# Kernel optimization log

Hardware: AMD Instinct MI355X
Metric: run time of the kernel (lower is better)

Reference implementation:

```python
import jax, jax.numpy as jnp
import numpy as np
from jax import lax

DIM = 512
HEADS = 8
N = 2048
B = 4
EPS = 1e-12  # torch F.normalize eps


def setup_inputs() -> dict:
    key = jax.random.key(0)
    ks = jax.random.split(key, 8)
    s = 0.02
    return {
        "x": jax.random.normal(ks[0], (B, DIM, N), jnp.float32),
        "w_qkv": jax.random.normal(ks[1], (3 * DIM, DIM, 1), jnp.float32) * s,
        "b_qkv": jax.random.normal(ks[2], (3 * DIM,), jnp.float32) * s,
        "w_dw": jax.random.normal(ks[3], (3 * DIM, 1, 3), jnp.float32) * s,
        "b_dw": jax.random.normal(ks[4], (3 * DIM,), jnp.float32) * s,
        "w_po": jax.random.normal(ks[5], (DIM, DIM, 1), jnp.float32) * s,
        "b_po": jax.random.normal(ks[6], (DIM,), jnp.float32) * s,
        "temperature": jnp.ones((HEADS, 1, 1), jnp.float32),
    }


def _l2norm(x, axis):
    n = jnp.sqrt(jnp.sum(x * x, axis=axis, keepdims=True))
    return x / jnp.maximum(n, EPS)


def reference(x, w_qkv, b_qkv, w_dw, b_dw, w_po, b_po, temperature):
    b, c, n = x.shape
    ch = c // HEADS
    # 1x1 conv (pointwise)
    qkv = jnp.einsum('oc,bcn->bon', w_qkv[:, :, 0], x) + b_qkv[None, :, None]
    # depthwise conv k=3, pad=1
    qkv = lax.conv_general_dilated(
        qkv, w_dw, window_strides=(1,), padding=[(1, 1)],
        dimension_numbers=('NCH', 'OIH', 'NCH'),
        feature_group_count=3 * c) + b_dw[None, :, None]
    q, k, v = jnp.split(qkv, 3, axis=1)  # each [b, c, n]
    q = q.reshape(b, HEADS, ch, n)
    k = k.reshape(b, HEADS, ch, n)
    v = v.reshape(b, HEADS, ch, n)
    q = _l2norm(q, axis=-1)          # normalize over sequence axis
    k = _l2norm(k, axis=1)           # normalize over HEAD axis (faithful)
    # attn[i, j] = sum_c k[c, i] * q[c, j]  -> [b, h, n, n]
    attn = jnp.einsum('bhci,bhcj->bhij', k, q) * temperature[None]
    attn = jax.nn.softmax(attn, axis=-1)
    out = jnp.einsum('bhij,bhcj->bhic', attn, v)  # [b, h, n, ch]
    out = out.transpose(0, 1, 3, 2).reshape(b, c, n)  # b (head c) n
    out = jnp.einsum('oc,bcn->bon', w_po[:, :, 0], out) + b_po[None, :, None]
    return out
```

## Files before the change

kernel.cpp:

```cpp
#include <hip/hip_runtime.h>
#include <hip/hip_bf16.h>

#define BATCH 4
#define DIM 512
#define HEADS 8
#define CH 64
#define SEQ 2048
#define C3 1536
#define L2EPS 1e-12f

typedef float f32x4 __attribute__((ext_vector_type(4)));
typedef short s16x8 __attribute__((ext_vector_type(8)));
typedef short s16x4 __attribute__((ext_vector_type(4)));
typedef unsigned short ushort_t;

static __device__ __forceinline__ unsigned bfpair(float a, float b) {
  unsigned ua = __builtin_bit_cast(unsigned, a);
  unsigned ub = __builtin_bit_cast(unsigned, b);
  ua = (ua + 0x7FFFu + ((ua >> 16) & 1u)) >> 16;
  ub = (ub + 0x7FFFu + ((ub >> 16) & 1u)) >> 16;
  return ua | (ub << 16);
}

static __device__ __forceinline__ unsigned cvtpk(float lo, float hi) {
  unsigned r;
  asm("v_cvt_pk_bf16_f32 %0, %1, %2" : "=v"(r) : "v"(lo), "v"(hi));
  return r;
}

static __device__ __forceinline__ float fexp2(float x) {
  float r;
  asm("v_exp_f32 %0, %1" : "=v"(r) : "v"(x));
  return r;
}

static __device__ __forceinline__ void gl_lds16(const void* g, void* l) {
  __builtin_amdgcn_global_load_lds(
      (const __attribute__((address_space(1))) unsigned int*)g,
      (__attribute__((address_space(3))) unsigned int*)l, 16, 0, 0);
}

__global__ __launch_bounds__(256) void wprep(
    const float* __restrict__ wq, const float* __restrict__ wp,
    unsigned* __restrict__ wqb, unsigned* __restrict__ wpb) {
  const int id = blockIdx.x * 256 + threadIdx.x;
  const float* src;
  unsigned* dst;
  int rid;
  if (id < 1536 * 256) { src = wq; dst = wqb; rid = id; }
  else                 { src = wp; dst = wpb; rid = id - 1536 * 256; }
  const int m = rid >> 8, dcol = rid & 255;
  const int chunk = dcol >> 5, dw = dcol & 31;
  const int sdw = chunk * 32 + (dw ^ (4 * (m & 7)));
  const float* s = src + (size_t)m * 512 + 2 * sdw;
  dst[rid] = bfpair(s[0], s[1]);
}

__global__ __launch_bounds__(256) void xpose_bf16(
    const float* __restrict__ x, unsigned* __restrict__ xbt) {
  __shared__ unsigned T[64][32];
  const int b = blockIdx.z;
  const int k0 = blockIdx.y * 64;
  const int n0 = blockIdx.x * 64;
  const int nl = threadIdx.x & 63;
  const int dwg = threadIdx.x >> 6;
  const float* xb = x + ((size_t)b * DIM + k0) * SEQ + n0 + nl;
#pragma unroll
  for (int dd = 0; dd < 8; ++dd) {
    const int dw = dwg * 8 + dd;
    const float v0 = xb[(size_t)(2 * dw) * SEQ];
    const float v1 = xb[(size_t)(2 * dw + 1) * SEQ];
    T[nl][dw ^ (4 * (nl & 7))] = bfpair(v0, v1);
  }
  __syncthreads();
#pragma unroll
  for (int rep = 0; rep < 8; ++rep) {
    const int id = rep * 256 + threadIdx.x;
    const int row = id >> 5, dw = id & 31;
    xbt[((size_t)b * SEQ + n0 + row) * 256 + (k0 >> 1) + dw] = T[row][dw];
  }
}

__global__ __launch_bounds__(256) void gemm_mfma_bf16(
    const ushort_t* __restrict__ Wb, const ushort_t* __restrict__ Bt,
    const float* __restrict__ bias, float* __restrict__ Y,
    int M, int N) {
  __shared__ __align__(16) char lds[32768];
  char* As = lds;
  char* Bs = lds + 16384;
  const int b = blockIdx.z;
  const int m0 = blockIdx.y * 128, n0 = blockIdx.x * 128;
  const int t = threadIdx.x, w = t >> 6, lane = t & 63;
  const int l15 = lane & 15, g = lane >> 4;
  const int key = 16 * (l15 & 7);
  const int wm = (w >> 1) * 64, wn = (w & 1) * 64;

  const int rsub = lane >> 3;
  const int csub = (lane & 7) * 8;

  f32x4 acc[4][4] = {};

  const ushort_t* Ag0 = Wb + (size_t)(m0 + 32 * w + rsub) * 512 + csub;
  const ushort_t* Bg0 = Bt + ((size_t)b * N + n0 + 32 * w + rsub) * 512 + csub;
  char* Al0 = As + (32 * w) * 128;
  char* Bl0 = Bs + (32 * w) * 128;

  for (int kc = 0; kc < 8; ++kc) {
    const int ko64 = kc * 64;
#pragma unroll
    for (int ri = 0; ri < 4; ++ri) {
      gl_lds16(Ag0 + (size_t)(8 * ri) * 512 + ko64, Al0 + ri * 1024);
      gl_lds16(Bg0 + (size_t)(8 * ri) * 512 + ko64, Bl0 + ri * 1024);
    }
    __syncthreads();
    const char* Abase = As + (wm + l15) * 128;
    const char* Bbase = Bs + (wn + l15) * 128;
#pragma unroll
    for (int ks = 0; ks < 2; ++ks) {
      const int ko = (64 * ks + 16 * g) ^ key;
      s16x8 af[4], bf[4];
#pragma unroll
      for (int mf = 0; mf < 4; ++mf) af[mf] = *(const s16x8*)(Abase + mf * 2048 + ko);
#pragma unroll
      for (int nf = 0; nf < 4; ++nf) bf[nf] = *(const s16x8*)(Bbase + nf * 2048 + ko);
#pragma unroll
      for (int mf = 0; mf < 4; ++mf)
#pragma unroll
        for (int nf = 0; nf < 4; ++nf)
          acc[mf][nf] = __builtin_amdgcn_mfma_f32_16x16x32_bf16(
              af[mf], bf[nf], acc[mf][nf], 0, 0, 0);
    }
    __syncthreads();
  }

#pragma unroll
  for (int mf = 0; mf < 4; ++mf) {
#pragma unroll
    for (int rg = 0; rg < 4; ++rg) {
      const int m = m0 + wm + 16 * mf + 4 * g + rg;
      const float bv = bias[m];
      float* yp = Y + ((size_t)b * M + m) * N + n0 + wn + l15;
#pragma unroll
      for (int nf = 0; nf < 4; ++nf)
        yp[16 * nf] = acc[mf][nf][rg] + bv;
    }
  }
}

__global__ __launch_bounds__(256) void dwconv2(
    const float* __restrict__ pre, const float* __restrict__ wdw,
    const float* __restrict__ bdw, float* __restrict__ qkv,
    unsigned* __restrict__ vb, float* __restrict__ rq) {
  __shared__ float red[4];
  const int row = blockIdx.x;
  const int o = row % C3;
  const int b = row / C3;
  const int n0 = threadIdx.x * 8;
  const float* src = pre + (size_t)row * SEQ + n0;
  float4 m0 = *(const float4*)src;
  float4 m1 = *(const float4*)(src + 4);
  const float left  = (n0 > 0) ? src[-1] : 0.f;
  const float right = (n0 < SEQ - 8) ? src[8] : 0.f;
  const float w0 = wdw[o * 3 + 0], w1 = wdw[o * 3 + 1], w2 = wdw[o * 3 + 2];
  const float bv = bdw[o];
  const float mid[8] = {m0.x, m0.y, m0.z, m0.w, m1.x, m1.y, m1.z, m1.w};
  const float lf[8]  = {left, m0.x, m0.y, m0.z, m0.w, m1.x, m1.y, m1.z};
  const float rt[8]  = {m0.y, m0.z, m0.w, m1.x, m1.y, m1.z, m1.w, right};
  float y[8];
#pragma unroll
  for (int u = 0; u < 8; ++u) y[u] = w0 * lf[u] + w1 * mid[u] + w2 * rt[u] + bv;

  if (o < 2 * DIM) {
    float* dst = qkv + (size_t)row * SEQ + n0;
    *(float4*)dst = make_float4(y[0], y[1], y[2], y[3]);
    *(float4*)(dst + 4) = make_float4(y[4], y[5], y[6], y[7]);
    if (o < DIM) {
      float s = 0.f;
#pragma unroll
      for (int u = 0; u < 8; ++u) s += y[u] * y[u];
#pragma unroll
      for (int off = 32; off > 0; off >>= 1) s += __shfl_down(s, off);
      if ((threadIdx.x & 63) == 0) red[threadIdx.x >> 6] = s;
      __syncthreads();
      if (threadIdx.x == 0) {
        const float tv = red[0] + red[1] + red[2] + red[3];
        rq[b * DIM + o] = 1.0f / fmaxf(sqrtf(tv), L2EPS);
      }
    }
  } else {
    const int oc = o - 2 * DIM;
    const int h = oc >> 6, cc = oc & 63;
    const int bh = b * 8 + h;
    const int jt = n0 >> 6, d0 = (n0 & 63) >> 1;
    uint4 pk;
    pk.x = bfpair(y[0], y[1]); pk.y = bfpair(y[2], y[3]);
    pk.z = bfpair(y[4], y[5]); pk.w = bfpair(y[6], y[7]);
    *(uint4*)&vb[((size_t)(bh * 32 + jt) * 64 + cc) * 32 +
                 (d0 ^ (4 * (cc & 7)))] = pk;
  }
}

__global__ __launch_bounds__(256) void knorm_kernel(
    const float* __restrict__ qkv, float* __restrict__ rk) {
  const int idx = blockIdx.x * 256 + threadIdx.x;
  const int n = idx & (SEQ - 1);
  const int cc = (idx >> 11) & 63;
  const int b = idx >> 17;
  const float* base = qkv + ((size_t)b * C3 + DIM + cc) * SEQ + n;
  float s = 0.f;
#pragma unroll
  for (int h = 0; h < HEADS; ++h) {
    float v = base[(size_t)h * CH * SEQ];
    s += v * v;
  }
  rk[idx] = 1.0f / fmaxf(sqrtf(s), L2EPS);
}

__global__ __launch_bounds__(256) void prep2(
    const float* __restrict__ qkv, const float* __restrict__ rq,
    const float* __restrict__ rk, const float* __restrict__ temp,
    unsigned* __restrict__ qt, unsigned* __restrict__ kt) {
  __shared__ unsigned T[64][32];
  const int jt = blockIdx.x, bh = blockIdx.y, sec = blockIdx.z;
  const int b = bh >> 3, h = bh & 7;
  const int jl = threadIdx.x & 63, dwg = threadIdx.x >> 6;
  const int j = jt * 64 + jl;
  if (sec == 0) {
    const float* base = qkv + ((size_t)b * C3 + h * CH) * SEQ + j;
    const float* rqb = rq + b * DIM + h * CH;
#pragma unroll
    for (int dd = 0; dd < 8; ++dd) {
      const int dw = dwg * 8 + dd;
      float v0 = base[(size_t)(2 * dw) * SEQ] * rqb[2 * dw];
      float v1 = base[(size_t)(2 * dw + 1) * SEQ] * rqb[2 * dw + 1];
      T[jl][dw ^ (4 * (jl & 7))] = bfpair(v0, v1);
    }
  } else {
    const float f = temp[h] * 1.44269504f;
    const float* base = qkv + ((size_t)b * C3 + DIM + h * CH) * SEQ + j;
    const float* rkb = rk + (size_t)b * CH * SEQ + j;
#pragma unroll
    for (int dd = 0; dd < 8; ++dd) {
      const int dw = dwg * 8 + dd;
      float v0 = base[(size_t)(2 * dw) * SEQ] * rkb[(size_t)(2 * dw) * SEQ] * f;
      float v1 = base[(size_t)(2 * dw + 1) * SEQ] * rkb[(size_t)(2 * dw + 1) * SEQ] * f;
      T[jl][dw] = bfpair(v0, v1);
    }
  }
  __syncthreads();
  unsigned* dst = (sec == 0 ? qt : kt) + ((size_t)bh * SEQ + jt * 64) * 32;
#pragma unroll
  for (int rep = 0; rep < 8; ++rep) {
    const int id = rep * 256 + threadIdx.x;
    dst[id] = T[id >> 5][id & 31];
  }
}

__global__ __launch_bounds__(256, 3) void flash_mfma(
    const ushort_t* __restrict__ qt, const ushort_t* __restrict__ kt,
    const ushort_t* __restrict__ vb, unsigned* __restrict__ attn_t) {
  __shared__ __align__(16) char lds[32768];
  char* const Q0 = lds;
  char* const Q1 = lds + 8192;
  char* const V0 = lds + 16384;
  char* const V1 = lds + 24576;

  const int orig = blockIdx.y * 32 + blockIdx.x;
  const int swz = (orig & 7) * 128 + (orig >> 3);
  const int bh = swz >> 5, b = bh >> 3, h = bh & 7;
  const int i0 = (swz & 31) * 64;

  const int t = threadIdx.x, w = t >> 6, lane = t & 63;
  const int l15 = lane & 15, g = lane >> 4;
  const int key = 16 * (lane & 7);

  const ushort_t* ktp = kt + ((size_t)bh * SEQ + i0 + l15) * 64 + 8 * g;
  s16x8 kf0[4], kf1[4];
#pragma unroll
  for (int ib = 0; ib < 4; ++ib) {
    kf0[ib] = *(const s16x8*)(ktp + ib * 1024);
    kf1[ib] = *(const s16x8*)(ktp + ib * 1024 + 32);
  }

  const ushort_t* qtile = qt + (size_t)bh * SEQ * 64;
  const ushort_t* vtile = vb + (size_t)bh * 32 * 4096;

  const int li0 = (w * 2) * 64 + lane;
  const int li1 = li0 + 64;
  const int wo = (w * 2) * 1024;

  const int qoff = (16 * w + l15) * 128;
  const int a0off = (16 * g) ^ key;
  const int a1off = (16 * g + 64) ^ key;
  const int voff = l15 * 128 + ((32 * w + 8 * g) ^ key);

  f32x4 accO[4][4] = {};
  float lr[4] = {};

#define FSTAGE(JT, QD, VD)                                               \
  do {                                                                   \
    gl_lds16(qtile + (size_t)(JT) * 4096 + li0 * 8, (QD) + wo);          \
    gl_lds16(qtile + (size_t)(JT) * 4096 + li1 * 8, (QD) + wo + 1024);   \
    gl_lds16(vtile + (size_t)(JT) * 4096 + li0 * 8, (VD) + wo);          \
    gl_lds16(vtile + (size_t)(JT) * 4096 + li1 * 8, (VD) + wo + 1024);   \
  } while (0)

  auto compute = [&](const char* Qs, const char* Vs) {
    const s16x8 a0 = *(const s16x8*)(Qs + qoff + a0off);
    const s16x8 a1 = *(const s16x8*)(Qs + qoff + a1off);
    s16x4 vf[4];
#pragma unroll
    for (int mf = 0; mf < 4; ++mf)
      vf[mf] = *(const s16x4*)(Vs + mf * 2048 + voff);

    f32x4 st[4];
    __builtin_amdgcn_s_setprio(1);
#pragma unroll
    for (int ib = 0; ib < 4; ++ib) {
      f32x4 z = {};
      z = __builtin_amdgcn_mfma_f32_16x16x32_bf16(a0, kf0[ib], z, 0, 0, 0);
      z = __builtin_amdgcn_mfma_f32_16x16x32_bf16(a1, kf1[ib], z, 0, 0, 0);
      st[ib] = z;
    }
    __builtin_amdgcn_s_setprio(0);

    s16x4 pb[4];
#pragma unroll
    for (int ib = 0; ib < 4; ++ib) {
      const float p0 = fexp2(st[ib][0]);
      const float p1 = fexp2(st[ib][1]);
      const float p2 = fexp2(st[ib][2]);
      const float p3 = fexp2(st[ib][3]);
      lr[ib] += (p0 + p1) + (p2 + p3);
      uint2 u;
      u.x = cvtpk(p0, p1);
      u.y = cvtpk(p2, p3);
      pb[ib] = __builtin_bit_cast(s16x4, u);
    }

    __builtin_amdgcn_s_setprio(1);
#pragma unroll
    for (int ib = 0; ib < 4; ++ib)
#pragma unroll
      for (int mf = 0; mf < 4; ++mf)
        accO[mf][ib] = __builtin_amdgcn_mfma_f32_16x16x16bf16_1k(
            vf[mf], pb[ib], accO[mf][ib], 0, 0, 0);
    __builtin_amdgcn_s_setprio(0);
  };

  FSTAGE(0, Q0, V0);
  __syncthreads();
#pragma unroll 1
  for (int jt2 = 0; jt2 < 16; ++jt2) {
    const int jt = 2 * jt2;
    FSTAGE(jt + 1, Q1, V1);
    compute(Q0, V0);
    __syncthreads();
    if (jt2 < 15) FSTAGE(jt + 2, Q0, V0);
    compute(Q1, V1);
    __syncthreads();
  }

  float* ldsL = (float*)(lds + 24576);
#pragma unroll
  for (int ib = 0; ib < 4; ++ib) {
    lr[ib] += __shfl_xor(lr[ib], 16);
    lr[ib] += __shfl_xor(lr[ib], 32);
  }
  if (lane < 16)
    *(float4*)(ldsL + (w * 16 + l15) * 4) =
        make_float4(lr[0], lr[1], lr[2], lr[3]);

  float* red = (float*)lds;
  f32x4 rAcc[4];
#pragma unroll
  for (int r = 0; r < 4; ++r) {
#pragma unroll
    for (int mf = 0; mf < 4; ++mf)
      *(f32x4*)(red + w * 1024 + lane * 16 + ((mf ^ (lane & 3)) * 4)) =
          accO[mf][r];
    __syncthreads();
    if (w == r) {
#pragma unroll
      for (int mf = 0; mf < 4; ++mf) {
        f32x4 s = {};
#pragma unroll
        for (int w2 = 0; w2 < 4; ++w2)
          s += *(const f32x4*)(red + w2 * 1024 + lane * 16 +
                               ((mf ^ (lane & 3)) * 4));
        rAcc[mf] = s;
      }
    }
    __syncthreads();
  }

  float lsum = 0.f;
#pragma unroll
  for (int w2 = 0; w2 < 4; ++w2) lsum += ldsL[(w2 * 16 + l15) * 4 + w];
  const float inv = 1.0f / lsum;

  unsigned* Pw = (unsigned*)(lds + 16384 + w * 2048);
  const int kk = 4 * (l15 & 7);
#pragma unroll
  for (int mf = 0; mf < 4; ++mf) {
    uint2 pk;
    pk.x = cvtpk(rAcc[mf][0] * inv, rAcc[mf][1] * inv);
    pk.y = cvtpk(rAcc[mf][2] * inv, rAcc[mf][3] * inv);
    const int dwb = 8 * mf + 2 * g;
    *(uint2*)&Pw[l15 * 32 + (dwb ^ kk)] = pk;
  }
  __syncthreads();
#pragma unroll
  for (int rep = 0; rep < 8; ++rep) {
    const int id = rep * 64 + lane;
    const int row = id >> 5, dw = id & 31;
    attn_t[((size_t)b * SEQ + i0 + 16 * w + row) * 256 + h * 32 + dw] =
        Pw[row * 32 + dw];
  }
}

extern "C" void kernel_launch(void* const* d_in, const int* in_sizes, int n_in,
                              void* d_out, int out_size, void* d_ws, size_t ws_size,
                              hipStream_t stream) {
  const float* x      = (const float*)d_in[0];
  const float* w_qkv  = (const float*)d_in[1];
  const float* b_qkv  = (const float*)d_in[2];
  const float* w_dw   = (const float*)d_in[3];
  const float* b_dw   = (const float*)d_in[4];
  const float* w_po   = (const float*)d_in[5];
  const float* b_po   = (const float*)d_in[6];
  const float* temp   = (const float*)d_in[7];
  float* out = (float*)d_out;
  float* ws  = (float*)d_ws;

  float* qkv_pre = ws;
  float* qkv     = ws + 12582912;
  float* rq      = ws + 25165824;
  float* rk      = ws + 25167872;
  unsigned* xbt  = (unsigned*)(ws + 25692160);
  unsigned* wqb  = (unsigned*)(ws + 27789312);
  unsigned* wpb  = (unsigned*)(ws + 28182528);
  unsigned* vb     = (unsigned*)(ws + 25692160);
  unsigned* qt     = (unsigned*)(ws);
  unsigned* kt     = (unsigned*)(ws + 2097152);
  unsigned* attn_t = (unsigned*)(ws + 4194304);

  wprep<<<2048, 256, 0, stream>>>(w_qkv, w_po, wqb, wpb);
  xpose_bf16<<<dim3(SEQ / 64, DIM / 64, BATCH), 256, 0, stream>>>(x, xbt);

  gemm_mfma_bf16<<<dim3(SEQ / 128, C3 / 128, BATCH), 256, 0, stream>>>(
      (const ushort_t*)wqb, (const ushort_t*)xbt, b_qkv, qkv_pre, C3, SEQ);

  dwconv2<<<BATCH * C3, 256, 0, stream>>>(qkv_pre, w_dw, b_dw, qkv, vb, rq);

  knorm_kernel<<<(BATCH * CH * SEQ) / 256, 256, 0, stream>>>(qkv, rk);

  prep2<<<dim3(32, BATCH * HEADS, 2), 256, 0, stream>>>(
      qkv, rq, rk, temp, qt, kt);

  flash_mfma<<<dim3(SEQ / 64, BATCH * HEADS), 256, 0, stream>>>(
      (const ushort_t*)qt, (const ushort_t*)kt, (const ushort_t*)vb, attn_t);

  gemm_mfma_bf16<<<dim3(SEQ / 128, DIM / 128, BATCH), 256, 0, stream>>>(
      (const ushort_t*)wpb, (const ushort_t*)attn_t, b_po, out, DIM, SEQ);
}
```

Measured before the change: 127.1 us.

## Triple-buffer Q/V tiles in flash kernel with vmcnt-based waits

```diff
diff --git a/kernel.cpp b/kernel.cpp
--- a/kernel.cpp
+++ b/kernel.cpp
@@ -259,11 +259,13 @@
 __global__ __launch_bounds__(256, 3) void flash_mfma(
     const ushort_t* __restrict__ qt, const ushort_t* __restrict__ kt,
     const ushort_t* __restrict__ vb, unsigned* __restrict__ attn_t) {
-  __shared__ __align__(16) char lds[32768];
+  __shared__ __align__(16) char lds[49152];
   char* const Q0 = lds;
   char* const Q1 = lds + 8192;
-  char* const V0 = lds + 16384;
-  char* const V1 = lds + 24576;
+  char* const Q2 = lds + 16384;
+  char* const V0 = lds + 24576;
+  char* const V1 = lds + 32768;
+  char* const V2 = lds + 40960;
 
   const int orig = blockIdx.y * 32 + blockIdx.x;
   const int swz = (orig & 7) * 128 + (orig >> 3);
@@ -303,6 +305,19 @@
     gl_lds16(qtile + (size_t)(JT) * 4096 + li1 * 8, (QD) + wo + 1024);   \
     gl_lds16(vtile + (size_t)(JT) * 4096 + li0 * 8, (VD) + wo);          \
     gl_lds16(vtile + (size_t)(JT) * 4096 + li1 * 8, (VD) + wo + 1024);   \
+  } while (0)
+
+#define PHASE4()                                         \
+  do {                                                   \
+    asm volatile("s_waitcnt vmcnt(4)" ::: "memory");     \
+    __builtin_amdgcn_s_barrier();                        \
+    __builtin_amdgcn_sched_barrier(0);                   \
+  } while (0)
+#define PHASE0()                                         \
+  do {                                                   \
+    asm volatile("s_waitcnt vmcnt(0)" ::: "memory");     \
+    __builtin_amdgcn_s_barrier();                        \
+    __builtin_amdgcn_sched_barrier(0);                   \
   } while (0)
 
   auto compute = [&](const char* Qs, const char* Vs) {
@@ -349,19 +364,18 @@
   };
 
   FSTAGE(0, Q0, V0);
-  __syncthreads();
+  FSTAGE(1, Q1, V1);
 #pragma unroll 1
-  for (int jt2 = 0; jt2 < 16; ++jt2) {
-    const int jt = 2 * jt2;
-    FSTAGE(jt + 1, Q1, V1);
-    compute(Q0, V0);
-    __syncthreads();
-    if (jt2 < 15) FSTAGE(jt + 2, Q0, V0);
-    compute(Q1, V1);
-    __syncthreads();
-  }
-
-  float* ldsL = (float*)(lds + 24576);
+  for (int tt = 0; tt < 10; ++tt) {
+    const int jt = 3 * tt;
+    PHASE4(); FSTAGE(jt + 2, Q2, V2); compute(Q0, V0);
+    PHASE4(); FSTAGE(jt + 3, Q0, V0); compute(Q1, V1);
+    PHASE4(); FSTAGE(jt + 4, Q1, V1); compute(Q2, V2);
+  }
+  PHASE4(); compute(Q0, V0);
+  PHASE0(); compute(Q1, V1);
+
+  float* ldsL = (float*)(lds + 40960);
 #pragma unroll
   for (int ib = 0; ib < 4; ++ib) {
     lr[ib] += __shfl_xor(lr[ib], 16);
@@ -370,6 +384,7 @@
   if (lane < 16)
     *(float4*)(ldsL + (w * 16 + l15) * 4) =
         make_float4(lr[0], lr[1], lr[2], lr[3]);
+  __syncthreads();
 
   float* red = (float*)lds;
   f32x4 rAcc[4];
@@ -417,6 +432,9 @@
     attn_t[((size_t)b * SEQ + i0 + 16 * w + row) * 256 + h * 32 + dw] =
         Pw[row * 32 + dw];
   }
+#undef FSTAGE
+#undef PHASE4
+#undef PHASE0
 }
 
 extern "C" void kernel_launch(void* const* d_in, const int* in_sizes, int n_in,
```

New measurement: 223.1 us. 1.76x slower.

## Load Q and V fragments directly from global into registers, dropping LDS staging

Applied to the files above, without the earlier changes.

```diff
diff --git a/kernel.cpp b/kernel.cpp
--- a/kernel.cpp
+++ b/kernel.cpp
@@ -258,12 +258,8 @@
 
 __global__ __launch_bounds__(256, 3) void flash_mfma(
     const ushort_t* __restrict__ qt, const ushort_t* __restrict__ kt,
-    const ushort_t* __restrict__ vb, unsigned* __restrict__ attn_t) {
-  __shared__ __align__(16) char lds[32768];
-  char* const Q0 = lds;
-  char* const Q1 = lds + 8192;
-  char* const V0 = lds + 16384;
-  char* const V1 = lds + 24576;
+    const unsigned* __restrict__ vb, unsigned* __restrict__ attn_t) {
+  __shared__ __align__(16) char lds[17408];
 
   const int orig = blockIdx.y * 32 + blockIdx.x;
   const int swz = (orig & 7) * 128 + (orig >> 3);
@@ -282,86 +278,83 @@
     kf1[ib] = *(const s16x8*)(ktp + ib * 1024 + 32);
   }
 
-  const ushort_t* qtile = qt + (size_t)bh * SEQ * 64;
-  const ushort_t* vtile = vb + (size_t)bh * 32 * 4096;
-
-  const int li0 = (w * 2) * 64 + lane;
-  const int li1 = li0 + 64;
-  const int wo = (w * 2) * 1024;
-
-  const int qoff = (16 * w + l15) * 128;
+  const char* qrow =
+      (const char*)qt + ((size_t)bh * SEQ + 16 * w + l15) * 128;
   const int a0off = (16 * g) ^ key;
   const int a1off = (16 * g + 64) ^ key;
-  const int voff = l15 * 128 + ((32 * w + 8 * g) ^ key);
+  const unsigned* vrow = vb + ((size_t)bh * 32 * 64 + l15) * 32 +
+                         ((8 * w + 2 * g) ^ (4 * (l15 & 7)));
 
   f32x4 accO[4][4] = {};
   float lr[4] = {};
 
-#define FSTAGE(JT, QD, VD)                                               \
-  do {                                                                   \
-    gl_lds16(qtile + (size_t)(JT) * 4096 + li0 * 8, (QD) + wo);          \
-    gl_lds16(qtile + (size_t)(JT) * 4096 + li1 * 8, (QD) + wo + 1024);   \
-    gl_lds16(vtile + (size_t)(JT) * 4096 + li0 * 8, (VD) + wo);          \
-    gl_lds16(vtile + (size_t)(JT) * 4096 + li1 * 8, (VD) + wo + 1024);   \
+  s16x8 qa0A, qa1A, qa0B, qa1B;
+  s16x4 vf0A, vf1A, vf2A, vf3A, vf0B, vf1B, vf2B, vf3B;
+
+#define LOADT(S, JT)                                                       \
+  do {                                                                     \
+    const char* qb = qrow + (size_t)(JT) * 8192;                           \
+    const unsigned* vbp = vrow + (size_t)(JT) * 2048;                      \
+    qa0##S = *(const s16x8*)(qb + a0off);                                  \
+    qa1##S = *(const s16x8*)(qb + a1off);                                  \
+    vf0##S = *(const s16x4*)(vbp);                                         \
+    vf1##S = *(const s16x4*)(vbp + 512);                                   \
+    vf2##S = *(const s16x4*)(vbp + 1024);                                  \
+    vf3##S = *(const s16x4*)(vbp + 1536);                                  \
   } while (0)
 
-  auto compute = [&](const char* Qs, const char* Vs) {
-    const s16x8 a0 = *(const s16x8*)(Qs + qoff + a0off);
-    const s16x8 a1 = *(const s16x8*)(Qs + qoff + a1off);
-    s16x4 vf[4];
-#pragma unroll
-    for (int mf = 0; mf < 4; ++mf)
-      vf[mf] = *(const s16x4*)(Vs + mf * 2048 + voff);
-
-    f32x4 st[4];
-    __builtin_amdgcn_s_setprio(1);
-#pragma unroll
-    for (int ib = 0; ib < 4; ++ib) {
-      f32x4 z = {};
-      z = __builtin_amdgcn_mfma_f32_16x16x32_bf16(a0, kf0[ib], z, 0, 0, 0);
-      z = __builtin_amdgcn_mfma_f32_16x16x32_bf16(a1, kf1[ib], z, 0, 0, 0);
-      st[ib] = z;
-    }
-    __builtin_amdgcn_s_setprio(0);
-
-    s16x4 pb[4];
-#pragma unroll
-    for (int ib = 0; ib < 4; ++ib) {
-      const float p0 = fexp2(st[ib][0]);
-      const float p1 = fexp2(st[ib][1]);
-      const float p2 = fexp2(st[ib][2]);
-      const float p3 = fexp2(st[ib][3]);
-      lr[ib] += (p0 + p1) + (p2 + p3);
-      uint2 u;
-      u.x = cvtpk(p0, p1);
-      u.y = cvtpk(p2, p3);
-      pb[ib] = __builtin_bit_cast(s16x4, u);
-    }
-
-    __builtin_amdgcn_s_setprio(1);
-#pragma unroll
-    for (int ib = 0; ib < 4; ++ib)
-#pragma unroll
-      for (int mf = 0; mf < 4; ++mf)
-        accO[mf][ib] = __builtin_amdgcn_mfma_f32_16x16x16bf16_1k(
-            vf[mf], pb[ib], accO[mf][ib], 0, 0, 0);
-    __builtin_amdgcn_s_setprio(0);
-  };
-
-  FSTAGE(0, Q0, V0);
-  __syncthreads();
+#define COMPUTE(S)                                                         \
+  do {                                                                     \
+    f32x4 st[4];                                                           \
+    __builtin_amdgcn_s_setprio(1);                                         \
+    _Pragma("unroll") for (int ib = 0; ib < 4; ++ib) {                     \
+      f32x4 z = {};                                                        \
+      z = __builtin_amdgcn_mfma_f32_16x16x32_bf16(qa0##S, kf0[ib], z, 0, 0, 0); \
+      z = __builtin_amdgcn_mfma_f32_16x16x32_bf16(qa1##S, kf1[ib], z, 0, 0, 0); \
+      st[ib] = z;                                                          \
+    }                                                                      \
+    __builtin_amdgcn_s_setprio(0);                                         \
+    s16x4 pb[4];                                                           \
+    _Pragma("unroll") for (int ib = 0; ib < 4; ++ib) {                     \
+      const float p0 = fexp2(st[ib][0]);                                   \
+      const float p1 = fexp2(st[ib][1]);                                   \
+      const float p2 = fexp2(st[ib][2]);                                   \
+      const float p3 = fexp2(st[ib][3]);                                   \
+      lr[ib] += (p0 + p1) + (p2 + p3);                                     \
+      uint2 u;                                                             \
+      u.x = cvtpk(p0, p1);                                                 \
+      u.y = cvtpk(p2, p3);                                                 \
+      pb[ib] = __builtin_bit_cast(s16x4, u);                               \
+    }                                                                      \
+    __builtin_amdgcn_s_setprio(1);                                         \
+    _Pragma("unroll") for (int ib = 0; ib < 4; ++ib) {                     \
+      accO[0][ib] = __builtin_amdgcn_mfma_f32_16x16x16bf16_1k(             \
+          vf0##S, pb[ib], accO[0][ib], 0, 0, 0);                           \
+      accO[1][ib] = __builtin_amdgcn_mfma_f32_16x16x16bf16_1k(             \
+          vf1##S, pb[ib], accO[1][ib], 0, 0, 0);                           \
+      accO[2][ib] = __builtin_amdgcn_mfma_f32_16x16x16bf16_1k(             \
+          vf2##S, pb[ib], accO[2][ib], 0, 0, 0);                           \
+      accO[3][ib] = __builtin_amdgcn_mfma_f32_16x16x16bf16_1k(             \
+          vf3##S, pb[ib], accO[3][ib], 0, 0, 0);                           \
+    }                                                                      \
+    __builtin_amdgcn_s_setprio(0);                                         \
+  } while (0)
+
+  LOADT(A, 0);
+  LOADT(B, 1);
 #pragma unroll 1
-  for (int jt2 = 0; jt2 < 16; ++jt2) {
-    const int jt = 2 * jt2;
-    FSTAGE(jt + 1, Q1, V1);
-    compute(Q0, V0);
-    __syncthreads();
-    if (jt2 < 15) FSTAGE(jt + 2, Q0, V0);
-    compute(Q1, V1);
-    __syncthreads();
-  }
-
-  float* ldsL = (float*)(lds + 24576);
+  for (int jt2 = 0; jt2 < 15; ++jt2) {
+    COMPUTE(A);
+    LOADT(A, 2 * jt2 + 2);
+    COMPUTE(B);
+    LOADT(B, 2 * jt2 + 3);
+  }
+  COMPUTE(A);
+  COMPUTE(B);
+#undef LOADT
+#undef COMPUTE
+
+  float* ldsL = (float*)(lds + 16384);
 #pragma unroll
   for (int ib = 0; ib < 4; ++ib) {
     lr[ib] += __shfl_xor(lr[ib], 16);
@@ -399,7 +392,7 @@
   for (int w2 = 0; w2 < 4; ++w2) lsum += ldsL[(w2 * 16 + l15) * 4 + w];
   const float inv = 1.0f / lsum;
 
-  unsigned* Pw = (unsigned*)(lds + 16384 + w * 2048);
+  unsigned* Pw = (unsigned*)(lds) + w * 512;
   const int kk = 4 * (l15 & 7);
 #pragma unroll
   for (int mf = 0; mf < 4; ++mf) {
@@ -459,7 +452,7 @@
       qkv, rq, rk, temp, qt, kt);
 
   flash_mfma<<<dim3(SEQ / 64, BATCH * HEADS), 256, 0, stream>>>(
-      (const ushort_t*)qt, (const ushort_t*)kt, (const ushort_t*)vb, attn_t);
+      (const ushort_t*)qt, (const ushort_t*)kt, (const unsigned*)vb, attn_t);
 
   gemm_mfma_bf16<<<dim3(SEQ / 128, DIM / 128, BATCH), 256, 0, stream>>>(
       (const ushort_t*)wpb, (const ushort_t*)attn_t, b_po, out, DIM, SEQ);
```

Result: slower. 132.0 us (+3.9%).

## Load Q/V fragments directly from global into registers, dropping LDS staging

Applied to the files above, without the earlier changes.

```diff
diff --git a/kernel.cpp b/kernel.cpp
--- a/kernel.cpp
+++ b/kernel.cpp
@@ -11,7 +11,6 @@
 
 typedef float f32x4 __attribute__((ext_vector_type(4)));
 typedef short s16x8 __attribute__((ext_vector_type(8)));
-typedef short s16x4 __attribute__((ext_vector_type(4)));
 typedef unsigned short ushort_t;
 
 static __device__ __forceinline__ unsigned bfpair(float a, float b) {
@@ -191,12 +190,11 @@
     const int oc = o - 2 * DIM;
     const int h = oc >> 6, cc = oc & 63;
     const int bh = b * 8 + h;
-    const int jt = n0 >> 6, d0 = (n0 & 63) >> 1;
+    const int jt = n0 >> 7, jl = n0 & 127;
     uint4 pk;
     pk.x = bfpair(y[0], y[1]); pk.y = bfpair(y[2], y[3]);
     pk.z = bfpair(y[4], y[5]); pk.w = bfpair(y[6], y[7]);
-    *(uint4*)&vb[((size_t)(bh * 32 + jt) * 64 + cc) * 32 +
-                 (d0 ^ (4 * (cc & 7)))] = pk;
+    *(uint4*)&vb[((size_t)(bh * 16 + jt) * 64 + cc) * 64 + (jl >> 1)] = pk;
   }
 }
 
@@ -244,7 +242,7 @@
       const int dw = dwg * 8 + dd;
       float v0 = base[(size_t)(2 * dw) * SEQ] * rkb[(size_t)(2 * dw) * SEQ] * f;
       float v1 = base[(size_t)(2 * dw + 1) * SEQ] * rkb[(size_t)(2 * dw + 1) * SEQ] * f;
-      T[jl][dw] = bfpair(v0, v1);
+      T[jl][dw ^ (4 * (jl & 7))] = bfpair(v0, v1);
     }
   }
   __syncthreads();
@@ -252,18 +250,21 @@
 #pragma unroll
   for (int rep = 0; rep < 8; ++rep) {
     const int id = rep * 256 + threadIdx.x;
-    dst[id] = T[id >> 5][id & 31];
-  }
-}
-
-__global__ __launch_bounds__(256, 3) void flash_mfma(
+    const int row = id >> 5, dw = id & 31;
+    const unsigned val = T[row][dw ^ (4 * (row & 7))];
+    int dstrow = row;
+    if (sec == 0) {
+      const int s = row >> 5, rl = row & 31;
+      dstrow = (s << 5) | (16 * ((rl >> 2) & 1) + 4 * (rl >> 3) + (rl & 3));
+    }
+    dst[dstrow * 32 + dw] = val;
+  }
+}
+
+__global__ __launch_bounds__(256, 2) void flash_mfma(
     const ushort_t* __restrict__ qt, const ushort_t* __restrict__ kt,
     const ushort_t* __restrict__ vb, unsigned* __restrict__ attn_t) {
-  __shared__ __align__(16) char lds[32768];
-  char* const Q0 = lds;
-  char* const Q1 = lds + 8192;
-  char* const V0 = lds + 16384;
-  char* const V1 = lds + 24576;
+  __shared__ __align__(16) char lds[17408];
 
   const int orig = blockIdx.y * 32 + blockIdx.x;
   const int swz = (orig & 7) * 128 + (orig >> 3);
@@ -272,7 +273,6 @@
 
   const int t = threadIdx.x, w = t >> 6, lane = t & 63;
   const int l15 = lane & 15, g = lane >> 4;
-  const int key = 16 * (lane & 7);
 
   const ushort_t* ktp = kt + ((size_t)bh * SEQ + i0 + l15) * 64 + 8 * g;
   s16x8 kf0[4], kf1[4];
@@ -282,86 +282,95 @@
     kf1[ib] = *(const s16x8*)(ktp + ib * 1024 + 32);
   }
 
-  const ushort_t* qtile = qt + (size_t)bh * SEQ * 64;
-  const ushort_t* vtile = vb + (size_t)bh * 32 * 4096;
-
-  const int li0 = (w * 2) * 64 + lane;
-  const int li1 = li0 + 64;
-  const int wo = (w * 2) * 1024;
-
-  const int qoff = (16 * w + l15) * 128;
-  const int a0off = (16 * g) ^ key;
-  const int a1off = (16 * g + 64) ^ key;
-  const int voff = l15 * 128 + ((32 * w + 8 * g) ^ key);
+  const ushort_t* qp = qt + ((size_t)bh * SEQ + 32 * w + l15) * 64 + 8 * g;
+  const ushort_t* vp =
+      vb + (((size_t)bh * 16) * 64 + l15) * 128 + 32 * w + 8 * g;
 
   f32x4 accO[4][4] = {};
   float lr[4] = {};
 
-#define FSTAGE(JT, QD, VD)                                               \
+  s16x8 qa00, qa01, qa10, qa11;
+  s16x8 vf0, vf1, vf2, vf3;
+
+#define QLOAD(JT)                                                        \
   do {                                                                   \
-    gl_lds16(qtile + (size_t)(JT) * 4096 + li0 * 8, (QD) + wo);          \
-    gl_lds16(qtile + (size_t)(JT) * 4096 + li1 * 8, (QD) + wo + 1024);   \
-    gl_lds16(vtile + (size_t)(JT) * 4096 + li0 * 8, (VD) + wo);          \
-    gl_lds16(vtile + (size_t)(JT) * 4096 + li1 * 8, (VD) + wo + 1024);   \
+    const ushort_t* qb = qp + (size_t)(JT) * 8192;                       \
+    qa00 = *(const s16x8*)(qb);                                          \
+    qa01 = *(const s16x8*)(qb + 32);                                     \
+    qa10 = *(const s16x8*)(qb + 1024);                                   \
+    qa11 = *(const s16x8*)(qb + 1056);                                   \
   } while (0)
-
-  auto compute = [&](const char* Qs, const char* Vs) {
-    const s16x8 a0 = *(const s16x8*)(Qs + qoff + a0off);
-    const s16x8 a1 = *(const s16x8*)(Qs + qoff + a1off);
-    s16x4 vf[4];
-#pragma unroll
-    for (int mf = 0; mf < 4; ++mf)
-      vf[mf] = *(const s16x4*)(Vs + mf * 2048 + voff);
-
-    f32x4 st[4];
+#define VLOAD(JT)                                                        \
+  do {                                                                   \
+    const ushort_t* vbp = vp + (size_t)(JT) * 8192;                      \
+    vf0 = *(const s16x8*)(vbp);                                          \
+    vf1 = *(const s16x8*)(vbp + 2048);                                   \
+    vf2 = *(const s16x8*)(vbp + 4096);                                   \
+    vf3 = *(const s16x8*)(vbp + 6144);                                   \
+  } while (0)
+
+  QLOAD(0);
+  VLOAD(0);
+#pragma unroll 1
+  for (int jt = 0; jt < 16; ++jt) {
+    f32x4 st0[4], st1[4];
     __builtin_amdgcn_s_setprio(1);
 #pragma unroll
     for (int ib = 0; ib < 4; ++ib) {
       f32x4 z = {};
-      z = __builtin_amdgcn_mfma_f32_16x16x32_bf16(a0, kf0[ib], z, 0, 0, 0);
-      z = __builtin_amdgcn_mfma_f32_16x16x32_bf16(a1, kf1[ib], z, 0, 0, 0);
-      st[ib] = z;
+      z = __builtin_amdgcn_mfma_f32_16x16x32_bf16(qa00, kf0[ib], z, 0, 0, 0);
+      z = __builtin_amdgcn_mfma_f32_16x16x32_bf16(qa01, kf1[ib], z, 0, 0, 0);
+      st0[ib] = z;
+    }
+#pragma unroll
+    for (int ib = 0; ib < 4; ++ib) {
+      f32x4 z = {};
+      z = __builtin_amdgcn_mfma_f32_16x16x32_bf16(qa10, kf0[ib], z, 0, 0, 0);
+      z = __builtin_amdgcn_mfma_f32_16x16x32_bf16(qa11, kf1[ib], z, 0, 0, 0);
+      st1[ib] = z;
     }
     __builtin_amdgcn_s_setprio(0);
-
-    s16x4 pb[4];
+    QLOAD(jt + 1);
+
+    s16x8 pb[4];
 #pragma unroll
     for (int ib = 0; ib < 4; ++ib) {
-      const float p0 = fexp2(st[ib][0]);
-      const float p1 = fexp2(st[ib][1]);
-      const float p2 = fexp2(st[ib][2]);
-      const float p3 = fexp2(st[ib][3]);
-      lr[ib] += (p0 + p1) + (p2 + p3);
-      uint2 u;
-      u.x = cvtpk(p0, p1);
-      u.y = cvtpk(p2, p3);
-      pb[ib] = __builtin_bit_cast(s16x4, u);
+      const float e0 = fexp2(st0[ib][0]);
+      const float e1 = fexp2(st0[ib][1]);
+      const float e2 = fexp2(st0[ib][2]);
+      const float e3 = fexp2(st0[ib][3]);
+      const float e4 = fexp2(st1[ib][0]);
+      const float e5 = fexp2(st1[ib][1]);
+      const float e6 = fexp2(st1[ib][2]);
+      const float e7 = fexp2(st1[ib][3]);
+      lr[ib] += ((e0 + e1) + (e2 + e3)) + ((e4 + e5) + (e6 + e7));
+      uint4 u;
+      u.x = cvtpk(e0, e1);
+      u.y = cvtpk(e2, e3);
+      u.z = cvtpk(e4, e5);
+      u.w = cvtpk(e6, e7);
+      pb[ib] = __builtin_bit_cast(s16x8, u);
     }
 
     __builtin_amdgcn_s_setprio(1);
 #pragma unroll
-    for (int ib = 0; ib < 4; ++ib)
-#pragma unroll
-      for (int mf = 0; mf < 4; ++mf)
-        accO[mf][ib] = __builtin_amdgcn_mfma_f32_16x16x16bf16_1k(
-            vf[mf], pb[ib], accO[mf][ib], 0, 0, 0);
+    for (int ib = 0; ib < 4; ++ib) {
+      accO[0][ib] = __builtin_amdgcn_mfma_f32_16x16x32_bf16(
+          vf0, pb[ib], accO[0][ib], 0, 0, 0);
+      accO[1][ib] = __builtin_amdgcn_mfma_f32_16x16x32_bf16(
+          vf1, pb[ib], accO[1][ib], 0, 0, 0);
+      accO[2][ib] = __builtin_amdgcn_mfma_f32_16x16x32_bf16(
+          vf2, pb[ib], accO[2][ib], 0, 0, 0);
+      accO[3][ib] = __builtin_amdgcn_mfma_f32_16x16x32_bf16(
+          vf3, pb[ib], accO[3][ib], 0, 0, 0);
+    }
     __builtin_amdgcn_s_setprio(0);
-  };
-
-  FSTAGE(0, Q0, V0);
-  __syncthreads();
-#pragma unroll 1
-  for (int jt2 = 0; jt2 < 16; ++jt2) {
-    const int jt = 2 * jt2;
-    FSTAGE(jt + 1, Q1, V1);
-    compute(Q0, V0);
-    __syncthreads();
-    if (jt2 < 15) FSTAGE(jt + 2, Q0, V0);
-    compute(Q1, V1);
-    __syncthreads();
-  }
-
-  float* ldsL = (float*)(lds + 24576);
+    VLOAD(jt + 1);
+  }
+#undef QLOAD
+#undef VLOAD
+
+  float* ldsL = (float*)(lds + 16384);
 #pragma unroll
   for (int ib = 0; ib < 4; ++ib) {
     lr[ib] += __shfl_xor(lr[ib], 16);
@@ -399,7 +408,7 @@
   for (int w2 = 0; w2 < 4; ++w2) lsum += ldsL[(w2 * 16 + l15) * 4 + w];
   const float inv = 1.0f / lsum;
 
-  unsigned* Pw = (unsigned*)(lds + 16384 + w * 2048);
+  unsigned* Pw = (unsigned*)(lds) + w * 512;
   const int kk = 4 * (l15 & 7);
 #pragma unroll
   for (int mf = 0; mf < 4; ++mf) {
```

After: 144.4 us. 13.6% more time.
